# Kernel tuning notes

Measured on AMD Instinct MI355X. Metric: run time of the kernel, lower is better.

The kernel has to match this reference:

```python
import jax, jax.numpy as jnp
import numpy as np

N_NODES = 100000
N_EDGES = 400000
IN_DIM, HID, OUT_DIM, NUM_REL = 768, 256, 128, 3


def _init_linear(key, fan_in, fan_out):
    k1, k2 = jax.random.split(key)
    s = 1.0 / np.sqrt(fan_in)
    W = jax.random.uniform(k1, (fan_in, fan_out), jnp.float32, -s, s)
    b = jax.random.uniform(k2, (fan_out,), jnp.float32, -s, s)
    return W, b


def setup_inputs() -> dict:
    key = jax.random.key(0)
    ks = jax.random.split(key, 12)
    x = jax.random.normal(ks[0], (N_NODES, IN_DIM), jnp.float32)
    edge_index = jax.random.randint(ks[1], (2, N_EDGES), 0, N_NODES, jnp.int64 if jax.config.jax_enable_x64 else jnp.int32).astype(jnp.int32)
    edge_type = jax.random.randint(ks[2], (N_EDGES,), 0, NUM_REL).astype(jnp.int32)
    W1, b1 = _init_linear(ks[3], IN_DIM, HID)
    s = 1.0 / np.sqrt(HID)
    conv1_W = jax.random.uniform(ks[4], (NUM_REL, HID, HID), jnp.float32, -s, s)
    conv1_root = jax.random.uniform(ks[5], (HID, HID), jnp.float32, -s, s)
    conv1_bias = jnp.zeros((HID,), jnp.float32)
    conv2_W = jax.random.uniform(ks[6], (NUM_REL, HID, HID), jnp.float32, -s, s)
    conv2_root = jax.random.uniform(ks[7], (HID, HID), jnp.float32, -s, s)
    conv2_bias = jnp.zeros((HID,), jnp.float32)
    W2, b2 = _init_linear(ks[8], HID, OUT_DIM)
    Wc, bc = _init_linear(ks[9], OUT_DIM, 2)
    return {"x": x, "edge_index": edge_index, "edge_type": edge_type,
            "batch_size": 1024,
            "W1": W1, "b1": b1,
            "conv1_W": conv1_W, "conv1_root": conv1_root, "conv1_bias": conv1_bias,
            "conv2_W": conv2_W, "conv2_root": conv2_root, "conv2_bias": conv2_bias,
            "W2": W2, "b2": b2, "Wc": Wc, "bc": bc}


def rgcn_conv(h, src, dst, edge_type, W, root, bias):
    # PyG RGCNConv: mean aggregation per relation + root transform + bias
    n = h.shape[0]
    hs = h[src]                                   # [E, HID] gather
    out = h @ root + bias                         # root/self term
    for r in range(NUM_REL):                      # fixed small relation count
        w = (edge_type == r).astype(h.dtype)      # [E]
        msg = (hs @ W[r]) * w[:, None]            # per-relation transform
        ssum = jax.ops.segment_sum(msg, dst, num_segments=n)
        cnt = jax.ops.segment_sum(w, dst, num_segments=n)
        out = out + ssum / jnp.maximum(cnt, 1.0)[:, None]
    return out


def reference(x, edge_index, edge_type, batch_size,
              W1, b1, conv1_W, conv1_root, conv1_bias,
              conv2_W, conv2_root, conv2_bias, W2, b2, Wc, bc):
    src, dst = edge_index[0], edge_index[1]
    h = jax.nn.relu(x @ W1 + b1)                  # linear1 + ReLU
    h = rgcn_conv(h, src, dst, edge_type, conv1_W, conv1_root, conv1_bias)
    # dropout: identity at inference
    h = rgcn_conv(h, src, dst, edge_type, conv2_W, conv2_root, conv2_bias)
    h = jax.nn.relu(h @ W2 + b2)                  # linear2 + ReLU
    logits = h @ Wc + bc                          # classifier
    return logits[:batch_size]
```

## Files before the change

kernel.cpp:

```cpp
#include <hip/hip_runtime.h>


#define N_NODES 100000
#define N_EDGES 400000
#define IN_DIM  768
#define HID     256
#define OUT_DIM 128
#define NREL    3
#define BATCH   1024
#define KCAT    1024
#define MSGW    768
#define CAP0    32768
#define CAP1    8192
#define ECAP1   32768
#define ECAP2   8192
#define NBAR    9
#define BLINES  64

typedef __attribute__((ext_vector_type(8))) short bf16x8;
typedef __attribute__((ext_vector_type(4))) float f32x4;

static __device__ __forceinline__ int imin(int a, int b) { return a < b ? a : b; }

static __device__ __forceinline__ unsigned short f2bf(float f) {
    union { float f; unsigned int u; } v; v.f = f;
    unsigned int r = v.u + 0x7FFFu + ((v.u >> 16) & 1u);
    return (unsigned short)(r >> 16);
}

struct Prm {
    const float* x; const int* ei; const int* et;
    const float *W1, *b1, *c1W, *c1root, *c1bias, *c2W, *c2root, *c2bias, *W2, *b2, *Wc, *bc;
    float* out;
    uint4* zp; int nz;
    int* bar;
    int *need1, *need0, *map1, *map0, *idx1, *idx0, *elist1, *elist2;
    int *n1ctr, *n0ctr, *ectr1, *ectr2;
    float *cnt1, *cnt2, *Amsg1, *Amsg2, *h0c, *h1c, *h2;
    unsigned short *w1s, *B1s, *B2s;
};

static __device__ __forceinline__ void gbar(int* bar, int slot) {
    __syncthreads();
    int* base = bar + slot * (BLINES * 16);
    if (threadIdx.x == 0) {
        __threadfence();
        atomicAdd(base + (blockIdx.x & (BLINES - 1)) * 16, 1);
    }
    if (threadIdx.x < BLINES) {
        int target = (int)(gridDim.x >> 6);
        int* line = base + threadIdx.x * 16;
        long spins = 0;
        while (__hip_atomic_load(line, __ATOMIC_ACQUIRE, __HIP_MEMORY_SCOPE_AGENT) < target) {
            __builtin_amdgcn_s_sleep(8);
            if (++spins > (1L << 20)) break;
        }
        __threadfence();
    }
    __syncthreads();
}


static __device__ void weight_prep_dev(const Prm& p, int gtid, int gstr) {
    const int P1n = (IN_DIM * HID) / 8, P2n = (KCAT * HID) / 8;
    for (int u = gtid; u < P1n + 2 * P2n; u += gstr) {
        unsigned int pk[4];
        if (u < P1n) {
            int base = u * 8;
            int j0 = base & 31, c = (base >> 5) & 255, s = base >> 13;
            #pragma unroll
            for (int q = 0; q < 4; q++) {
                unsigned short lo = f2bf(p.W1[((s * 32 + j0 + 2 * q) << 8) + c]);
                unsigned short hi = f2bf(p.W1[((s * 32 + j0 + 2 * q + 1) << 8) + c]);
                pk[q] = (unsigned int)lo | ((unsigned int)hi << 16);
            }
            *(uint4*)&p.w1s[base] = make_uint4(pk[0], pk[1], pk[2], pk[3]);
        } else {
            int which2 = (u - P1n) >= P2n;
            const float* root = which2 ? p.c2root : p.c1root;
            const float* Wr   = which2 ? p.c2W : p.c1W;
            unsigned short* dst = which2 ? p.B2s : p.B1s;
            int base = ((u - P1n) - (which2 ? P2n : 0)) * 8;
            int j0 = base & 31, c = (base >> 5) & 255, s = base >> 13;
            int k0 = s * 32 + j0;
            #pragma unroll
            for (int q = 0; q < 4; q++) {
                int ka = k0 + 2 * q, kb = ka + 1;
                float va = (ka < HID) ? root[(ka << 8) + c] : Wr[((ka - HID) << 8) + c];
                float vb = (kb < HID) ? root[(kb << 8) + c] : Wr[((kb - HID) << 8) + c];
                pk[q] = (unsigned int)f2bf(va) | ((unsigned int)f2bf(vb) << 16);
            }
            *(uint4*)&dst[base] = make_uint4(pk[0], pk[1], pk[2], pk[3]);
        }
    }
}

static __device__ void scatter_dev(const int* __restrict__ ei, const int* __restrict__ et,
                                   const int* __restrict__ elist, const int* __restrict__ ectr, int ecap,
                                   const int* __restrict__ mapSrc, const int* __restrict__ mapDst,
                                   const float* __restrict__ hsrc,
                                   float* __restrict__ Amsg, float* __restrict__ cnt,
                                   int cntStride, int gtid, int gstr) {
    int n = imin(*ectr, ecap);
    int tot = n * 64;
    for (int g = gtid; g < tot; g += gstr) {
        int ii = g >> 6, lane = g & 63;
        int e = elist[ii];
        int d = ei[N_EDGES + e];
        int row = mapDst ? mapDst[d] : d;
        if (row < 0) continue;
        int s = mapSrc[ei[e]];
        if (s < 0) continue;
        int r = et[e];
        float4 v = *(const float4*)(hsrc + (size_t)s * HID + lane * 4);
        float* dp = Amsg + (size_t)row * MSGW + (size_t)r * HID + lane * 4;
        atomicAdd(dp + 0, v.x);
        atomicAdd(dp + 1, v.y);
        atomicAdd(dp + 2, v.z);
        atomicAdd(dp + 3, v.w);
        if (lane == 0) atomicAdd(cnt + (size_t)r * cntStride + row, 1.0f);
    }
}

static __device__ void gemm1_tile(const float* __restrict__ x, const int* __restrict__ idx0,
                                  const unsigned short* __restrict__ w1s, const float* __restrict__ b1,
                                  float* __restrict__ h0c, int bm, int M,
                                  unsigned short (*As)[40], unsigned short (*Bs)[40]) {
    int tid = threadIdx.x;
    int w = tid >> 6, lane = tid & 63;
    int l16 = lane & 15, lhi = lane >> 4;
    int ar = tid >> 2, ac = tid & 3;
    int gr = idx0[imin(bm + ar, M - 1)];
    const float* aptr = x + (size_t)gr * IN_DIM + ac * 8;

    f32x4 acc[16];
    #pragma unroll
    for (int i = 0; i < 16; i++) acc[i] = (f32x4)0.0f;

    for (int k0 = 0; k0 < IN_DIM; k0 += 32) {
        float4 a0 = *(const float4*)(aptr + k0);
        float4 a1 = *(const float4*)(aptr + k0 + 4);
        unsigned int p0 = (unsigned int)f2bf(a0.x) | ((unsigned int)f2bf(a0.y) << 16);
        unsigned int p1 = (unsigned int)f2bf(a0.z) | ((unsigned int)f2bf(a0.w) << 16);
        unsigned int p2 = (unsigned int)f2bf(a1.x) | ((unsigned int)f2bf(a1.y) << 16);
        unsigned int p3 = (unsigned int)f2bf(a1.z) | ((unsigned int)f2bf(a1.w) << 16);
        *(uint4*)&As[ar][ac * 8] = make_uint4(p0, p1, p2, p3);

        const uint4* bsrc = (const uint4*)(w1s + ((size_t)(k0 >> 5) * 256 + tid) * 32);
        int bswz = (tid >> 3) & 3;
        uint4 b0 = bsrc[0], b1v = bsrc[1], b2 = bsrc[2], b3 = bsrc[3];
        *(uint4*)&Bs[tid][(0 ^ bswz) * 8] = b0;
        *(uint4*)&Bs[tid][(1 ^ bswz) * 8] = b1v;
        *(uint4*)&Bs[tid][(2 ^ bswz) * 8] = b2;
        *(uint4*)&Bs[tid][(3 ^ bswz) * 8] = b3;
        __syncthreads();

        bf16x8 af = *(bf16x8*)&As[w * 16 + l16][lhi * 8];
        #pragma unroll
        for (int f = 0; f < 16; f++) {
            int col = f * 16 + l16;
            bf16x8 bf = *(bf16x8*)&Bs[col][(lhi ^ ((col >> 3) & 3)) * 8];
            acc[f] = __builtin_amdgcn_mfma_f32_16x16x32_bf16(af, bf, acc[f], 0, 0, 0);
        }
        __syncthreads();
    }

    #pragma unroll
    for (int f = 0; f < 16; f++) {
        int col = f * 16 + l16;
        float bb = b1[col];
        #pragma unroll
        for (int reg = 0; reg < 4; reg++) {
            int row = bm + w * 16 + lhi * 4 + reg;
            if (row < M) h0c[(size_t)row * HID + col] = fmaxf(acc[f][reg] + bb, 0.0f);
        }
    }
}

static __device__ void conv_tile(const float* __restrict__ hsrc,
                                 const int* __restrict__ idx, const int* __restrict__ map,
                                 const float* __restrict__ Amsg,
                                 const float* __restrict__ cnt, int cntStride,
                                 const unsigned short* __restrict__ Bt, const float* __restrict__ bias,
                                 float* __restrict__ Cout, int bm, int M,
                                 unsigned short (*As)[40], unsigned short (*Bs)[40]) {
    int tid = threadIdx.x;
    int w = tid >> 6, lane = tid & 63;
    int l16 = lane & 15, lhi = lane >> 4;
    int ar = tid >> 2, ac = tid & 3;
    int row = imin(bm + ar, M - 1);
    int node = idx ? idx[row] : row;
    int grow = map[node]; if (grow < 0) grow = 0;
    const float* rootp = hsrc + (size_t)grow * HID + ac * 8;
    const float* msgp  = Amsg + (size_t)row * MSGW + ac * 8;
    float sc[NREL];
    #pragma unroll
    for (int r = 0; r < NREL; r++)
        sc[r] = 1.0f / fmaxf(cnt[(size_t)r * cntStride + row], 1.0f);

    f32x4 acc[16];
    #pragma unroll
    for (int i = 0; i < 16; i++) acc[i] = (f32x4)0.0f;

    for (int k0 = 0; k0 < KCAT; k0 += 32) {
        float4 a0, a1;
        if (k0 < HID) {
            a0 = *(const float4*)(rootp + k0);
            a1 = *(const float4*)(rootp + k0 + 4);
        } else {
            float s = sc[(k0 - HID) >> 8];
            a0 = *(const float4*)(msgp + (k0 - HID));
            a1 = *(const float4*)(msgp + (k0 - HID) + 4);
            a0.x *= s; a0.y *= s; a0.z *= s; a0.w *= s;
            a1.x *= s; a1.y *= s; a1.z *= s; a1.w *= s;
        }
        unsigned int p0 = (unsigned int)f2bf(a0.x) | ((unsigned int)f2bf(a0.y) << 16);
        unsigned int p1 = (unsigned int)f2bf(a0.z) | ((unsigned int)f2bf(a0.w) << 16);
        unsigned int p2 = (unsigned int)f2bf(a1.x) | ((unsigned int)f2bf(a1.y) << 16);
        unsigned int p3 = (unsigned int)f2bf(a1.z) | ((unsigned int)f2bf(a1.w) << 16);
        *(uint4*)&As[ar][ac * 8] = make_uint4(p0, p1, p2, p3);

        const uint4* bsrc = (const uint4*)(Bt + ((size_t)(k0 >> 5) * 256 + tid) * 32);
        int bswz = (tid >> 3) & 3;
        uint4 b0 = bsrc[0], b1v = bsrc[1], b2 = bsrc[2], b3 = bsrc[3];
        *(uint4*)&Bs[tid][(0 ^ bswz) * 8] = b0;
        *(uint4*)&Bs[tid][(1 ^ bswz) * 8] = b1v;
        *(uint4*)&Bs[tid][(2 ^ bswz) * 8] = b2;
        *(uint4*)&Bs[tid][(3 ^ bswz) * 8] = b3;
        __syncthreads();

        bf16x8 af = *(bf16x8*)&As[w * 16 + l16][lhi * 8];
        #pragma unroll
        for (int f = 0; f < 16; f++) {
            int col = f * 16 + l16;
            bf16x8 bf = *(bf16x8*)&Bs[col][(lhi ^ ((col >> 3) & 3)) * 8];
            acc[f] = __builtin_amdgcn_mfma_f32_16x16x32_bf16(af, bf, acc[f], 0, 0, 0);
        }
        __syncthreads();
    }

    #pragma unroll
    for (int f = 0; f < 16; f++) {
        int col = f * 16 + l16;
        float bb = bias[col];
        #pragma unroll
        for (int reg = 0; reg < 4; reg++) {
            int r = bm + w * 16 + lhi * 4 + reg;
            if (r < M) Cout[(size_t)r * HID + col] = acc[f][reg] + bb;
        }
    }
}

static __device__ void lin2_tile(const float* __restrict__ h2, const float* __restrict__ W2,
                                 const float* __restrict__ b2, const float* __restrict__ Wc,
                                 const float* __restrict__ bc, float* __restrict__ out, int bm,
                                 float (*Asf)[36], float (*Bsf)[132]) {
    int tid = threadIdx.x;
    int tx = tid & 15, ty = tid >> 4;
    int brow = tid >> 4, bch = tid & 15;

    float acc[2][8] = {};

    for (int k0 = 0; k0 < HID; k0 += 16) {
        if (tid < 128) {
            int arow = tid >> 2, ach = tid & 3;
            float4 av = *(const float4*)(h2 + (size_t)(bm + arow) * HID + k0 + ach * 4);
            Asf[ach * 4 + 0][arow] = av.x;
            Asf[ach * 4 + 1][arow] = av.y;
            Asf[ach * 4 + 2][arow] = av.z;
            Asf[ach * 4 + 3][arow] = av.w;
        }
        const float* bp = W2 + (size_t)(k0 + brow) * OUT_DIM;
        *(float4*)&Bsf[brow][bch * 4]      = *(const float4*)(bp + bch * 4);
        *(float4*)&Bsf[brow][64 + bch * 4] = *(const float4*)(bp + 64 + bch * 4);
        __syncthreads();
        #pragma unroll
        for (int k = 0; k < 16; k++) {
            float a0 = Asf[k][ty * 2], a1 = Asf[k][ty * 2 + 1];
            float4 b0 = *(const float4*)&Bsf[k][tx * 8];
            float4 b1 = *(const float4*)&Bsf[k][tx * 8 + 4];
            acc[0][0] += a0 * b0.x; acc[0][1] += a0 * b0.y; acc[0][2] += a0 * b0.z; acc[0][3] += a0 * b0.w;
            acc[0][4] += a0 * b1.x; acc[0][5] += a0 * b1.y; acc[0][6] += a0 * b1.z; acc[0][7] += a0 * b1.w;
            acc[1][0] += a1 * b0.x; acc[1][1] += a1 * b0.y; acc[1][2] += a1 * b0.z; acc[1][3] += a1 * b0.w;
            acc[1][4] += a1 * b1.x; acc[1][5] += a1 * b1.y; acc[1][6] += a1 * b1.z; acc[1][7] += a1 * b1.w;
        }
        __syncthreads();
    }

    float s0[2] = {0.f, 0.f}, s1[2] = {0.f, 0.f};
    #pragma unroll
    for (int j = 0; j < 8; j++) {
        int col = tx * 8 + j;
        float w0 = Wc[col * 2 + 0], w1 = Wc[col * 2 + 1];
        float bb = b2[col];
        #pragma unroll
        for (int i = 0; i < 2; i++) {
            float h = fmaxf(acc[i][j] + bb, 0.0f);
            s0[i] += h * w0;
            s1[i] += h * w1;
        }
    }
    #pragma unroll
    for (int o = 1; o <= 8; o <<= 1) {
        #pragma unroll
        for (int i = 0; i < 2; i++) {
            s0[i] += __shfl_xor(s0[i], o);
            s1[i] += __shfl_xor(s1[i], o);
        }
    }
    if (tx == 0) {
        #pragma unroll
        for (int i = 0; i < 2; i++) {
            int row = bm + ty * 2 + i;
            out[row * 2 + 0] = s0[i] + bc[0];
            out[row * 2 + 1] = s1[i] + bc[1];
        }
    }
}


__global__ __launch_bounds__(256, 2) void mega(Prm p) {
    __shared__ __align__(16) char sm[(64 * 40 + 256 * 40) * 2];
    unsigned short (*As)[40] = (unsigned short(*)[40])sm;
    unsigned short (*Bs)[40] = (unsigned short(*)[40])(sm + 64 * 40 * 2);

    const int tid  = threadIdx.x;
    const int gtid = blockIdx.x * 256 + tid;
    const int gstr = gridDim.x * 256;

    for (int e = gtid; e < N_EDGES; e += gstr) {
        if (p.ei[N_EDGES + e] < BATCH) {
            p.need1[p.ei[e]] = 1;
            int q = atomicAdd(p.ectr2, 1);
            if (q < ECAP2) p.elist2[q] = e;
        }
    }
    weight_prep_dev(p, gtid, gstr);
    gbar(p.bar, 0);

    for (int e = gtid; e < N_EDGES; e += gstr) {
        int d = p.ei[N_EDGES + e];
        if (d < BATCH || p.need1[d]) {
            p.need0[p.ei[e]] = 1;
            int q = atomicAdd(p.ectr1, 1);
            if (q < ECAP1) p.elist1[q] = e;
        }
    }
    {
        uint4 z = make_uint4(0u, 0u, 0u, 0u);
        for (int t = gtid; t < p.nz; t += gstr) p.zp[t] = z;
    }
    gbar(p.bar, 1);

    for (int i = gtid; i < N_NODES; i += gstr) {
        int f1 = (i < BATCH) | p.need1[i];
        int f0 = f1 | p.need0[i];
        if (f1) {
            int q = atomicAdd(p.n1ctr, 1);
            if (q < CAP1) { p.idx1[q] = i; p.map1[i] = q; } else p.map1[i] = -1;
        } else p.map1[i] = -1;
        if (f0) {
            int q = atomicAdd(p.n0ctr, 1);
            if (q < CAP0) { p.idx0[q] = i; p.map0[i] = q; } else p.map0[i] = -1;
        } else p.map0[i] = -1;
    }
    gbar(p.bar, 2);

    {
        int M = imin(*p.n0ctr, CAP0);
        int nt = (M + 63) >> 6;
        for (int t = blockIdx.x; t < nt; t += gridDim.x)
            gemm1_tile(p.x, p.idx0, p.w1s, p.b1, p.h0c, t * 64, M, As, Bs);
    }
    gbar(p.bar, 3);

    scatter_dev(p.ei, p.et, p.elist1, p.ectr1, ECAP1, p.map0, p.map1, p.h0c,
                p.Amsg1, p.cnt1, CAP1, gtid, gstr);
    gbar(p.bar, 4);

    {
        int M = imin(*p.n1ctr, CAP1);
        int nt = (M + 63) >> 6;
        for (int t = blockIdx.x; t < nt; t += gridDim.x)
            conv_tile(p.h0c, p.idx1, p.map0, p.Amsg1, p.cnt1, CAP1,
                      p.B1s, p.c1bias, p.h1c, t * 64, M, As, Bs);
    }
    gbar(p.bar, 5);

    scatter_dev(p.ei, p.et, p.elist2, p.ectr2, ECAP2, p.map1, nullptr, p.h1c,
                p.Amsg2, p.cnt2, BATCH, gtid, gstr);
    gbar(p.bar, 6);

    for (int t = blockIdx.x; t < BATCH / 64; t += gridDim.x)
        conv_tile(p.h1c, nullptr, p.map1, p.Amsg2, p.cnt2, BATCH,
                  p.B2s, p.c2bias, p.h2, t * 64, BATCH, As, Bs);
    gbar(p.bar, 7);

    {
        float (*Asf)[36]  = (float(*)[36])sm;
        float (*Bsf)[132] = (float(*)[132])(sm + 16 * 36 * 4);
        for (int t = blockIdx.x; t < BATCH / 32; t += gridDim.x)
            lin2_tile(p.h2, p.W2, p.b2, p.Wc, p.bc, p.out, t * 32, Asf, Bsf);
    }
}


__global__ void fb_zero_prep(Prm p) {
    int t = blockIdx.x * blockDim.x + threadIdx.x;
    if (t < p.nz) { p.zp[t] = make_uint4(0u, 0u, 0u, 0u); return; }
    weight_prep_dev(p, t - p.nz, 1 << 30);
}
__global__ void fb_mark1c(Prm p) {
    int e = blockIdx.x * blockDim.x + threadIdx.x;
    if (e >= N_EDGES) return;
    if (p.ei[N_EDGES + e] < BATCH) {
        p.need1[p.ei[e]] = 1;
        int q = atomicAdd(p.ectr2, 1);
        if (q < ECAP2) p.elist2[q] = e;
    }
}
__global__ void fb_mark0c(Prm p) {
    int e = blockIdx.x * blockDim.x + threadIdx.x;
    if (e >= N_EDGES) return;
    int d = p.ei[N_EDGES + e];
    if (d < BATCH || p.need1[d]) {
        p.need0[p.ei[e]] = 1;
        int q = atomicAdd(p.ectr1, 1);
        if (q < ECAP1) p.elist1[q] = e;
    }
}
__global__ void fb_compact(Prm p) {
    int i = blockIdx.x * blockDim.x + threadIdx.x;
    if (i >= N_NODES) return;
    int f1 = (i < BATCH) | p.need1[i];
    int f0 = f1 | p.need0[i];
    if (f1) {
        int q = atomicAdd(p.n1ctr, 1);
        if (q < CAP1) { p.idx1[q] = i; p.map1[i] = q; } else p.map1[i] = -1;
    } else p.map1[i] = -1;
    if (f0) {
        int q = atomicAdd(p.n0ctr, 1);
        if (q < CAP0) { p.idx0[q] = i; p.map0[i] = q; } else p.map0[i] = -1;
    } else p.map0[i] = -1;
}
__global__ __launch_bounds__(256) void fb_gemm1(Prm p) {
    __shared__ unsigned short As[64][40];
    __shared__ unsigned short Bs[256][40];
    int M = imin(*p.n0ctr, CAP0);
    int bm = blockIdx.x * 64;
    if (bm >= M) return;
    gemm1_tile(p.x, p.idx0, p.w1s, p.b1, p.h0c, bm, M, As, Bs);
}
__global__ void fb_scatter1(Prm p) {
    int g = blockIdx.x * blockDim.x + threadIdx.x;
    scatter_dev(p.ei, p.et, p.elist1, p.ectr1, ECAP1, p.map0, p.map1, p.h0c,
                p.Amsg1, p.cnt1, CAP1, g, 1 << 30);
}
__global__ __launch_bounds__(256) void fb_conv1(Prm p) {
    __shared__ unsigned short As[64][40];
    __shared__ unsigned short Bs[256][40];
    int M = imin(*p.n1ctr, CAP1);
    int bm = blockIdx.x * 64;
    if (bm >= M) return;
    conv_tile(p.h0c, p.idx1, p.map0, p.Amsg1, p.cnt1, CAP1, p.B1s, p.c1bias, p.h1c, bm, M, As, Bs);
}
__global__ void fb_scatter2(Prm p) {
    int g = blockIdx.x * blockDim.x + threadIdx.x;
    scatter_dev(p.ei, p.et, p.elist2, p.ectr2, ECAP2, p.map1, nullptr, p.h1c,
                p.Amsg2, p.cnt2, BATCH, g, 1 << 30);
}
__global__ __launch_bounds__(256) void fb_conv2(Prm p) {
    __shared__ unsigned short As[64][40];
    __shared__ unsigned short Bs[256][40];
    conv_tile(p.h1c, nullptr, p.map1, p.Amsg2, p.cnt2, BATCH, p.B2s, p.c2bias, p.h2,
              blockIdx.x * 64, BATCH, As, Bs);
}
__global__ __launch_bounds__(256) void fb_lin2(Prm p) {
    __shared__ float Asf[16][36];
    __shared__ float Bsf[16][132];
    lin2_tile(p.h2, p.W2, p.b2, p.Wc, p.bc, p.out, blockIdx.x * 32, Asf, Bsf);
}


extern "C" void kernel_launch(void* const* d_in, const int* in_sizes, int n_in,
                              void* d_out, int out_size, void* d_ws, size_t ws_size,
                              hipStream_t stream) {
    Prm p;
    p.x      = (const float*)d_in[0];
    p.ei     = (const int*)d_in[1];
    p.et     = (const int*)d_in[2];
    p.W1     = (const float*)d_in[4];
    p.b1     = (const float*)d_in[5];
    p.c1W    = (const float*)d_in[6];
    p.c1root = (const float*)d_in[7];
    p.c1bias = (const float*)d_in[8];
    p.c2W    = (const float*)d_in[9];
    p.c2root = (const float*)d_in[10];
    p.c2bias = (const float*)d_in[11];
    p.W2     = (const float*)d_in[12];
    p.b2     = (const float*)d_in[13];
    p.Wc     = (const float*)d_in[14];
    p.bc     = (const float*)d_in[15];
    p.out    = (float*)d_out;

    char* ws = (char*)d_ws;
    size_t off = 0;
    auto alloc = [&](size_t bytes) -> char* {
        char* q = ws + off;
        off = (off + bytes + 255) & ~(size_t)255;
        return q;
    };

    p.bar = (int*)alloc((size_t)NBAR * BLINES * 64);
    size_t zb_ctr  = 16;
    size_t zb_cnt1 = (size_t)NREL * CAP1 * 4;
    size_t zb_cnt2 = (size_t)NREL * BATCH * 4;
    size_t zb_need = (size_t)N_NODES * 4;
    char* zsmall = alloc(zb_ctr + zb_cnt1 + zb_cnt2 + 2 * zb_need);
    p.n1ctr = (int*)zsmall;
    p.n0ctr = p.n1ctr + 1;
    p.ectr1 = p.n1ctr + 2;
    p.ectr2 = p.n1ctr + 3;
    p.cnt1  = (float*)(zsmall + zb_ctr);
    p.cnt2  = (float*)(zsmall + zb_ctr + zb_cnt1);
    p.need1 = (int*)(zsmall + zb_ctr + zb_cnt1 + zb_cnt2);
    p.need0 = (int*)((char*)p.need1 + zb_need);
    size_t msbytes = (size_t)(((char*)p.need0 + zb_need) - (char*)p.bar);

    size_t zb_amsg1 = (size_t)CAP1 * MSGW * 4;
    size_t zb_amsg2 = (size_t)BATCH * MSGW * 4;
    char* amsg = alloc(zb_amsg1 + zb_amsg2);
    p.zp    = (uint4*)amsg;
    p.nz    = (int)((zb_amsg1 + zb_amsg2) / 16);
    p.Amsg1 = (float*)amsg;
    p.Amsg2 = (float*)(amsg + zb_amsg1);

    p.map1   = (int*)alloc(N_NODES * 4);
    p.map0   = (int*)alloc(N_NODES * 4);
    p.idx1   = (int*)alloc(CAP1 * 4);
    p.idx0   = (int*)alloc(CAP0 * 4);
    p.elist1 = (int*)alloc(ECAP1 * 4);
    p.elist2 = (int*)alloc(ECAP2 * 4);
    p.h0c    = (float*)alloc((size_t)CAP0 * HID * 4);
    p.h1c    = (float*)alloc((size_t)CAP1 * HID * 4);
    p.h2     = (float*)alloc((size_t)BATCH * HID * 4);
    p.w1s    = (unsigned short*)alloc((size_t)IN_DIM * HID * 2);
    p.B1s    = (unsigned short*)alloc((size_t)KCAT * HID * 2);
    p.B2s    = (unsigned short*)alloc((size_t)KCAT * HID * 2);
    (void)ws_size; (void)in_sizes; (void)n_in; (void)out_size;

    hipMemsetAsync(p.bar, 0, msbytes, stream);

    int occ = 0;
    hipError_t qe = hipOccupancyMaxActiveBlocksPerMultiprocessor(&occ, mega, 256, 0);

    if (qe == hipSuccess && occ >= 1) {
        int nblk = (occ >= 2) ? 512 : 256;
        mega<<<dim3(nblk), dim3(256), 0, stream>>>(p);
    } else {
        const int NB = 256;
        int prep_threads = (IN_DIM * HID) / 8 + 2 * (KCAT * HID) / 8;
        int zp_total = p.nz + prep_threads;
        fb_zero_prep<<<dim3((zp_total + NB - 1) / NB), NB, 0, stream>>>(p);
        fb_mark1c<<<dim3((N_EDGES + NB - 1) / NB), NB, 0, stream>>>(p);
        fb_mark0c<<<dim3((N_EDGES + NB - 1) / NB), NB, 0, stream>>>(p);
        fb_compact<<<dim3((N_NODES + NB - 1) / NB), NB, 0, stream>>>(p);
        fb_gemm1<<<dim3(CAP0 / 64), NB, 0, stream>>>(p);
        fb_scatter1<<<dim3(ECAP1 * 64 / NB), NB, 0, stream>>>(p);
        fb_conv1<<<dim3(CAP1 / 64), NB, 0, stream>>>(p);
        fb_scatter2<<<dim3(ECAP2 * 64 / NB), NB, 0, stream>>>(p);
        fb_conv2<<<dim3(BATCH / 64), NB, 0, stream>>>(p);
        fb_lin2<<<dim3(BATCH / 32), NB, 0, stream>>>(p);
    }
}
```

Before: 467.9 us.

## Replace global barriers with hierarchical per-XCD arrival counters

Each block reads its XCD id from a hardware register and registers itself per XCD once at startup. After the first full barrier, the remaining grid barriers become two-level: blocks increment a per-XCD arrival counter, and the last arriver in each XCD bumps a single done counter that all blocks poll. The aim is to cut the atomic traffic and polling contention of the 64-line barrier, and the sleep interval is shortened. It relies on the s_getreg XCC_ID encoding and on per-XCD counts, with a fallback when fewer than two XCDs are active.

```diff
diff --git a/kernel.cpp b/kernel.cpp
--- a/kernel.cpp
+++ b/kernel.cpp
@@ -14,8 +14,12 @@
 #define CAP1    8192
 #define ECAP1   32768
 #define ECAP2   8192
-#define NBAR    9
-#define BLINES  64
+
+#define FULL_OFF  0
+#define XCNT_OFF  1024
+#define ARR_OFF   1152
+#define DONE_OFF  2048
+#define BAR_INTS  2176
 
 typedef __attribute__((ext_vector_type(8))) short bf16x8;
 typedef __attribute__((ext_vector_type(4))) float f32x4;
@@ -40,22 +44,54 @@
     unsigned short *w1s, *B1s, *B2s;
 };
 
-static __device__ __forceinline__ void gbar(int* bar, int slot) {
+static __device__ __forceinline__ void gbar_full(int* bar) {
     __syncthreads();
-    int* base = bar + slot * (BLINES * 16);
+    int* base = bar + FULL_OFF;
     if (threadIdx.x == 0) {
         __threadfence();
-        atomicAdd(base + (blockIdx.x & (BLINES - 1)) * 16, 1);
-    }
-    if (threadIdx.x < BLINES) {
+        atomicAdd(base + (blockIdx.x & 63) * 16, 1);
+    }
+    if (threadIdx.x < 64) {
         int target = (int)(gridDim.x >> 6);
         int* line = base + threadIdx.x * 16;
         long spins = 0;
         while (__hip_atomic_load(line, __ATOMIC_ACQUIRE, __HIP_MEMORY_SCOPE_AGENT) < target) {
-            __builtin_amdgcn_s_sleep(8);
-            if (++spins > (1L << 20)) break;
+            __builtin_amdgcn_s_sleep(4);
+            if (++spins > (1L << 22)) break;
         }
         __threadfence();
+    }
+    __syncthreads();
+}
+
+static __device__ __forceinline__ void gbar_fast(int* bar, int slot, int xcd,
+                                                 int cntMy, int nAct) {
+    __syncthreads();
+    if (threadIdx.x == 0) {
+        int* done = bar + DONE_OFF + slot * 16;
+        if (nAct >= 2) {
+            int* arr = bar + ARR_OFF + (slot * 8 + xcd) * 16;
+            int a = atomicAdd(arr, 1) + 1;
+            if (a == cntMy) {
+                __builtin_amdgcn_fence(__ATOMIC_RELEASE, "agent");
+                atomicAdd(done, 1);
+            }
+            long spins = 0;
+            while (__hip_atomic_load(done, __ATOMIC_RELAXED, __HIP_MEMORY_SCOPE_AGENT) < nAct) {
+                __builtin_amdgcn_s_sleep(4);
+                if (++spins > (1L << 22)) break;
+            }
+            __builtin_amdgcn_fence(__ATOMIC_ACQUIRE, "agent");
+        } else {
+            __threadfence();
+            atomicAdd(done, 1);
+            long spins = 0;
+            while (__hip_atomic_load(done, __ATOMIC_ACQUIRE, __HIP_MEMORY_SCOPE_AGENT) < (int)gridDim.x) {
+                __builtin_amdgcn_s_sleep(4);
+                if (++spins > (1L << 22)) break;
+            }
+            __threadfence();
+        }
     }
     __syncthreads();
 }
@@ -323,10 +359,19 @@
     __shared__ __align__(16) char sm[(64 * 40 + 256 * 40) * 2];
     unsigned short (*As)[40] = (unsigned short(*)[40])sm;
     unsigned short (*Bs)[40] = (unsigned short(*)[40])(sm + 64 * 40 * 2);
+    __shared__ int s_xcd, s_cnt, s_nact;
 
     const int tid  = threadIdx.x;
     const int gtid = blockIdx.x * 256 + tid;
     const int gstr = gridDim.x * 256;
+
+    if (tid == 0) {
+        unsigned x = __builtin_amdgcn_s_getreg((31 << 11) | 20) & 7u;
+        s_xcd = (int)x;
+        atomicAdd(p.bar + XCNT_OFF + (int)x * 16, 1);
+    }
+    __syncthreads();
+    const int xcd = s_xcd;
 
     for (int e = gtid; e < N_EDGES; e += gstr) {
         if (p.ei[N_EDGES + e] < BATCH) {
@@ -336,7 +381,20 @@
         }
     }
     weight_prep_dev(p, gtid, gstr);
-    gbar(p.bar, 0);
+    gbar_full(p.bar);
+
+    if (tid == 0) {
+        int na = 0, cm = 0;
+        #pragma unroll
+        for (int k = 0; k < 8; k++) {
+            int c = p.bar[XCNT_OFF + k * 16];
+            na += (c > 0);
+            if (k == xcd) cm = c;
+        }
+        s_cnt = cm; s_nact = na;
+    }
+    __syncthreads();
+    const int cntMy = s_cnt, nAct = s_nact;
 
     for (int e = gtid; e < N_EDGES; e += gstr) {
         int d = p.ei[N_EDGES + e];
@@ -350,7 +408,7 @@
         uint4 z = make_uint4(0u, 0u, 0u, 0u);
         for (int t = gtid; t < p.nz; t += gstr) p.zp[t] = z;
     }
-    gbar(p.bar, 1);
+    gbar_fast(p.bar, 0, xcd, cntMy, nAct);
 
     for (int i = gtid; i < N_NODES; i += gstr) {
         int f1 = (i < BATCH) | p.need1[i];
@@ -364,7 +422,7 @@
             if (q < CAP0) { p.idx0[q] = i; p.map0[i] = q; } else p.map0[i] = -1;
         } else p.map0[i] = -1;
     }
-    gbar(p.bar, 2);
+    gbar_fast(p.bar, 1, xcd, cntMy, nAct);
 
     {
         int M = imin(*p.n0ctr, CAP0);
@@ -372,11 +430,11 @@
         for (int t = blockIdx.x; t < nt; t += gridDim.x)
             gemm1_tile(p.x, p.idx0, p.w1s, p.b1, p.h0c, t * 64, M, As, Bs);
     }
-    gbar(p.bar, 3);
+    gbar_fast(p.bar, 2, xcd, cntMy, nAct);
 
     scatter_dev(p.ei, p.et, p.elist1, p.ectr1, ECAP1, p.map0, p.map1, p.h0c,
                 p.Amsg1, p.cnt1, CAP1, gtid, gstr);
-    gbar(p.bar, 4);
+    gbar_fast(p.bar, 3, xcd, cntMy, nAct);
 
     {
         int M = imin(*p.n1ctr, CAP1);
@@ -385,16 +443,16 @@
             conv_tile(p.h0c, p.idx1, p.map0, p.Amsg1, p.cnt1, CAP1,
                       p.B1s, p.c1bias, p.h1c, t * 64, M, As, Bs);
     }
-    gbar(p.bar, 5);
+    gbar_fast(p.bar, 4, xcd, cntMy, nAct);
 
     scatter_dev(p.ei, p.et, p.elist2, p.ectr2, ECAP2, p.map1, nullptr, p.h1c,
                 p.Amsg2, p.cnt2, BATCH, gtid, gstr);
-    gbar(p.bar, 6);
+    gbar_fast(p.bar, 5, xcd, cntMy, nAct);
 
     for (int t = blockIdx.x; t < BATCH / 64; t += gridDim.x)
         conv_tile(p.h1c, nullptr, p.map1, p.Amsg2, p.cnt2, BATCH,
                   p.B2s, p.c2bias, p.h2, t * 64, BATCH, As, Bs);
-    gbar(p.bar, 7);
+    gbar_fast(p.bar, 6, xcd, cntMy, nAct);
 
     {
         float (*Asf)[36]  = (float(*)[36])sm;
@@ -511,7 +569,7 @@
         return q;
     };
 
-    p.bar = (int*)alloc((size_t)NBAR * BLINES * 64);
+    p.bar = (int*)alloc((size_t)BAR_INTS * 4);
     size_t zb_ctr  = 16;
     size_t zb_cnt1 = (size_t)NREL * CAP1 * 4;
     size_t zb_cnt2 = (size_t)NREL * BATCH * 4;
```

Result: no change. 467.2 us (-0.2%).
